# Kernel optimization log

Hardware: AMD Instinct MI355X
Metric: run time of the kernel (lower is better)

## Reference

```python
import jax, jax.numpy as jnp
import numpy as np

BN_EPS = 1e-5

def setup_inputs() -> dict:
    key = jax.random.key(0)
    k1, k2, k3 = jax.random.split(key, 3)
    N, T, C = 20000, 35, 4
    cin, cout = 7, 128
    h = cout // 2  # 64
    voxels = jax.random.normal(k1, (N, T, C), dtype=jnp.float32)
    # Linear params (torch default init scale ~ 1/sqrt(cin))
    W = jax.random.normal(k2, (h, cin), dtype=jnp.float32) / np.sqrt(cin)
    b = jax.random.normal(k3, (h,), dtype=jnp.float32) * 0.01
    gamma = jnp.ones((h,), dtype=jnp.float32)
    beta = jnp.zeros((h,), dtype=jnp.float32)
    return {"voxels": voxels, "W": W, "b": b, "gamma": gamma, "beta": beta}

def reference(voxels, W, b, gamma, beta):
    N, T, C = voxels.shape
    # mask of non-empty points: rows whose channel-sum is nonzero
    mask = (voxels.sum(axis=-1, keepdims=True) != 0)              # [N,T,1]
    counts = mask.sum(axis=1, keepdims=True).astype(voxels.dtype)  # [N,1,1]
    voxels_mean = voxels.sum(axis=1, keepdims=True) / counts       # [N,1,C]
    rel = voxels[:, :, :3] - voxels_mean[:, :, :3]                 # [N,T,3]
    aug = jnp.concatenate([voxels, rel], axis=-1)                  # [N,T,C+3]
    x = aug.reshape(-1, aug.shape[-1])                             # [N*T, 7]
    # Linear
    x = x @ W.T + b                                                # [N*T, h]
    # BatchNorm1d (training mode: batch stats, biased variance)
    mu = x.mean(axis=0)
    var = jnp.mean(jnp.square(x - mu), axis=0)
    x = (x - mu) / jnp.sqrt(var + BN_EPS) * gamma + beta
    # ReLU
    x = jnp.maximum(x, 0.0)
    x = x.reshape(N, T, -1)                                        # [N,T,h]
    agg = x.max(axis=1, keepdims=True)                             # [N,1,h]
    out = jnp.concatenate([x, jnp.broadcast_to(agg, x.shape)], axis=-1)  # [N,T,2h]
    return out
```

## Files before the change

### kernel.cpp

```cpp
#include <hip/hip_runtime.h>


#define NVOX   20000
#define TDIM   35
#define NCH    128
#define HID    64
#define NTF    700000.0f
#define EPS    1e-5f
#define NBLK_A 256
#define PARAM_OFF (NBLK_A * 35)

__global__ __launch_bounds__(256) void vfe_stats(const float* __restrict__ vox,
                                                 float* __restrict__ ws) {
  const int lane = threadIdx.x & 63;
  const int wid  = threadIdx.x >> 6;
  const int gwave  = (blockIdx.x * 256 + threadIdx.x) >> 6;
  const int nwaves = NBLK_A * 4;

  float m2[28], sv[7];
#pragma unroll
  for (int i = 0; i < 28; ++i) m2[i] = 0.f;
#pragma unroll
  for (int i = 0; i < 7; ++i) sv[i] = 0.f;

  for (int n = gwave; n < NVOX; n += nwaves) {
    float4 row = make_float4(0.f, 0.f, 0.f, 0.f);
    if (lane < TDIM) row = *(const float4*)(vox + (size_t)n * (TDIM * 4) + lane * 4);
    float rowsum = (row.x + row.y) + (row.z + row.w);
    float cnt = (float)__popcll(__ballot((lane < TDIM) && (rowsum != 0.f)));
    float s0 = row.x, s1 = row.y, s2 = row.z;
#pragma unroll
    for (int off = 32; off; off >>= 1) {
      s0 += __shfl_down(s0, off);
      s1 += __shfl_down(s1, off);
      s2 += __shfl_down(s2, off);
    }
    float rc = 1.f / cnt;
    float mx = __shfl(s0, 0) * rc;
    float my = __shfl(s1, 0) * rc;
    float mz = __shfl(s2, 0) * rc;
    if (lane < TDIM) {
      float a[7] = {row.x, row.y, row.z, row.w, row.x - mx, row.y - my, row.z - mz};
      int idx = 0;
#pragma unroll
      for (int j = 0; j < 7; ++j) {
        sv[j] += a[j];
#pragma unroll
        for (int k = j; k < 7; ++k) { m2[idx] = fmaf(a[j], a[k], m2[idx]); ++idx; }
      }
    }
  }

  __shared__ float part[4][35];
#pragma unroll
  for (int i = 0; i < 35; ++i) {
    float v = (i < 28) ? m2[i] : sv[i - 28];
#pragma unroll
    for (int off = 32; off; off >>= 1) v += __shfl_down(v, off);
    if (lane == 0) part[wid][i] = v;
  }
  __syncthreads();
  if (threadIdx.x < 35)
    ws[blockIdx.x * 35 + threadIdx.x] =
        part[0][threadIdx.x] + part[1][threadIdx.x] +
        part[2][threadIdx.x] + part[3][threadIdx.x];
}

__global__ void vfe_bnparams(const float* __restrict__ W, const float* __restrict__ b,
                             const float* __restrict__ gamma, const float* __restrict__ beta,
                             float* __restrict__ ws) {
  __shared__ float stats[35];
  for (int i = threadIdx.x; i < 35; i += 64) {
    float acc = 0.f;
    for (int p = 0; p < NBLK_A; ++p) acc += ws[p * 35 + i];
    stats[i] = acc;
  }
  __syncthreads();

  const int c = threadIdx.x;
  float m2[7][7];
  {
    int idx = 0;
    for (int j = 0; j < 7; ++j)
      for (int k = j; k < 7; ++k) { float v = stats[idx++]; m2[j][k] = v; m2[k][j] = v; }
  }
  float w[7];
#pragma unroll
  for (int j = 0; j < 7; ++j) w[j] = W[c * 7 + j];
  float bc = b[c];

  float wdots = 0.f;
#pragma unroll
  for (int j = 0; j < 7; ++j) wdots = fmaf(w[j], stats[28 + j], wdots);
  float q = 0.f;
#pragma unroll
  for (int j = 0; j < 7; ++j) {
    float t = 0.f;
#pragma unroll
    for (int k = 0; k < 7; ++k) t = fmaf(w[k], m2[j][k], t);
    q = fmaf(w[j], t, q);
  }
  float sx  = wdots + NTF * bc;
  float sxx = q + 2.f * bc * wdots + NTF * bc * bc;
  float mu  = sx / NTF;
  float var = sxx / NTF - mu * mu;
  float scale = gamma[c] / sqrtf(var + EPS);
  float shift = beta[c] + scale * (bc - mu);

  float* p = ws + PARAM_OFF + c * 8;
  p[0] = scale * (w[0] + w[4]);
  p[1] = scale * (w[1] + w[5]);
  p[2] = scale * (w[2] + w[6]);
  p[3] = scale * w[3];
  p[4] = scale * w[4];
  p[5] = scale * w[5];
  p[6] = scale * w[6];
  p[7] = shift;
}

__global__ __launch_bounds__(256) void vfe_encode(const float* __restrict__ vox,
                                                  const float* __restrict__ ws,
                                                  float* __restrict__ out) {
  const int lane = threadIdx.x & 63;
  const int wid  = threadIdx.x >> 6;
  const int n = (blockIdx.x * 256 + threadIdx.x) >> 6;

  __shared__ float4 rows[4][64];

  float4 row = make_float4(0.f, 0.f, 0.f, 0.f);
  if (lane < TDIM) row = *(const float4*)(vox + (size_t)n * (TDIM * 4) + lane * 4);
  float rowsum = (row.x + row.y) + (row.z + row.w);
  float cnt = (float)__popcll(__ballot((lane < TDIM) && (rowsum != 0.f)));
  float s0 = row.x, s1 = row.y, s2 = row.z;
#pragma unroll
  for (int off = 32; off; off >>= 1) {
    s0 += __shfl_down(s0, off);
    s1 += __shfl_down(s1, off);
    s2 += __shfl_down(s2, off);
  }
  float rc = 1.f / cnt;
  const float mx = __shfl(s0, 0) * rc;
  const float my = __shfl(s1, 0) * rc;
  const float mz = __shfl(s2, 0) * rc;

  rows[wid][lane] = row;
  __syncthreads();

  const int tg = lane >> 4;
  const int c4 = (lane & 15) << 2;

  const float4* pars = (const float4*)(ws + PARAM_OFF);
  float4 wv[4], wr[4];
  float base[4], agg[4];
#pragma unroll
  for (int i = 0; i < 4; ++i) {
    wv[i] = pars[(c4 + i) * 2];
    wr[i] = pars[(c4 + i) * 2 + 1];
    base[i] = wr[i].w - (wr[i].x * mx + wr[i].y * my + wr[i].z * mz);
    agg[i] = 0.f;
  }

  float* op = out + (size_t)n * (TDIM * NCH);
#pragma unroll
  for (int k = 0; k < 9; ++k) {
    const int t = 4 * k + tg;
    if (t < TDIM) {
      float4 v = rows[wid][t];
      float y[4];
#pragma unroll
      for (int i = 0; i < 4; ++i) {
        float d = fmaf(wv[i].x, v.x, base[i]);
        d = fmaf(wv[i].y, v.y, d);
        d = fmaf(wv[i].z, v.z, d);
        d = fmaf(wv[i].w, v.w, d);
        d = fmaxf(d, 0.f);
        agg[i] = fmaxf(agg[i], d);
        y[i] = d;
      }
      *(float4*)(op + t * NCH + c4) = make_float4(y[0], y[1], y[2], y[3]);
    }
  }

#pragma unroll
  for (int i = 0; i < 4; ++i) {
    agg[i] = fmaxf(agg[i], __shfl_xor(agg[i], 16));
    agg[i] = fmaxf(agg[i], __shfl_xor(agg[i], 32));
  }
  const float4 av = make_float4(agg[0], agg[1], agg[2], agg[3]);
#pragma unroll
  for (int k = 0; k < 9; ++k) {
    const int t = 4 * k + tg;
    if (t < TDIM) *(float4*)(op + t * NCH + HID + c4) = av;
  }
}

extern "C" void kernel_launch(void* const* d_in, const int* in_sizes, int n_in,
                              void* d_out, int out_size, void* d_ws, size_t ws_size,
                              hipStream_t stream) {
  const float* vox   = (const float*)d_in[0];
  const float* W     = (const float*)d_in[1];
  const float* b     = (const float*)d_in[2];
  const float* gamma = (const float*)d_in[3];
  const float* beta  = (const float*)d_in[4];
  float* out = (float*)d_out;
  float* ws  = (float*)d_ws;

  vfe_stats<<<NBLK_A, 256, 0, stream>>>(vox, ws);
  vfe_bnparams<<<1, 64, 0, stream>>>(W, b, gamma, beta, ws);
  vfe_encode<<<NVOX / 4, 256, 0, stream>>>(vox, ws, out);
}
```

Baseline: 407.7 us.

## Prefetch rows in stats loop, parallelize BN reduction, use nontemporal output stores

The stats kernel now software-prefetches the next voxel row while the current row is being processed, so load latency overlaps with compute. Partial statistics are stored transposed so the single-block bnparams kernel can reduce them with 280 threads using float4 loads, where before 35 threads did serial loops. The encode kernel writes its large output with nontemporal stores to avoid polluting the cache. The costs are extra registers for the prefetch and a dependence on how the hardware handles nontemporal stores.

```diff
diff --git a/kernel.cpp b/kernel.cpp
--- a/kernel.cpp
+++ b/kernel.cpp
@@ -10,6 +10,8 @@
 #define NBLK_A 256
 #define PARAM_OFF (NBLK_A * 35)
 
+typedef float nt4 __attribute__((ext_vector_type(4)));
+
 __global__ __launch_bounds__(256) void vfe_stats(const float* __restrict__ vox,
                                                  float* __restrict__ ws) {
   const int lane = threadIdx.x & 63;
@@ -23,9 +25,15 @@
 #pragma unroll
   for (int i = 0; i < 7; ++i) sv[i] = 0.f;
 
+  float4 row = make_float4(0.f, 0.f, 0.f, 0.f);
+  if (lane < TDIM) row = *(const float4*)(vox + (size_t)gwave * (TDIM * 4) + lane * 4);
+
   for (int n = gwave; n < NVOX; n += nwaves) {
-    float4 row = make_float4(0.f, 0.f, 0.f, 0.f);
-    if (lane < TDIM) row = *(const float4*)(vox + (size_t)n * (TDIM * 4) + lane * 4);
+    const int nn = n + nwaves;
+    float4 nxt = make_float4(0.f, 0.f, 0.f, 0.f);
+    if (nn < NVOX && lane < TDIM)
+      nxt = *(const float4*)(vox + (size_t)nn * (TDIM * 4) + lane * 4);
+
     float rowsum = (row.x + row.y) + (row.z + row.w);
     float cnt = (float)__popcll(__ballot((lane < TDIM) && (rowsum != 0.f)));
     float s0 = row.x, s1 = row.y, s2 = row.z;
@@ -49,6 +57,7 @@
         for (int k = j; k < 7; ++k) { m2[idx] = fmaf(a[j], a[k], m2[idx]); ++idx; }
       }
     }
+    row = nxt;
   }
 
   __shared__ float part[4][35];
@@ -61,23 +70,41 @@
   }
   __syncthreads();
   if (threadIdx.x < 35)
-    ws[blockIdx.x * 35 + threadIdx.x] =
+    ws[threadIdx.x * NBLK_A + blockIdx.x] =
         part[0][threadIdx.x] + part[1][threadIdx.x] +
         part[2][threadIdx.x] + part[3][threadIdx.x];
 }
 
-__global__ void vfe_bnparams(const float* __restrict__ W, const float* __restrict__ b,
+__global__ __launch_bounds__(320) void vfe_bnparams(const float* __restrict__ W,
+                             const float* __restrict__ b,
                              const float* __restrict__ gamma, const float* __restrict__ beta,
                              float* __restrict__ ws) {
+  __shared__ float part[35][8];
   __shared__ float stats[35];
-  for (int i = threadIdx.x; i < 35; i += 64) {
+  const int tid = threadIdx.x;
+
+  if (tid < 280) {
+    const int i = tid >> 3, g = tid & 7;
+    const float4* src = (const float4*)(ws + i * NBLK_A + g * 32);
     float acc = 0.f;
-    for (int p = 0; p < NBLK_A; ++p) acc += ws[p * 35 + i];
-    stats[i] = acc;
-  }
-  __syncthreads();
-
-  const int c = threadIdx.x;
+#pragma unroll
+    for (int q = 0; q < 8; ++q) {
+      float4 v = src[q];
+      acc += (v.x + v.y) + (v.z + v.w);
+    }
+    part[i][g] = acc;
+  }
+  __syncthreads();
+  if (tid < 35) {
+    float a = 0.f;
+#pragma unroll
+    for (int g = 0; g < 8; ++g) a += part[tid][g];
+    stats[tid] = a;
+  }
+  __syncthreads();
+  if (tid >= 64) return;
+
+  const int c = tid;
   float m2[7][7];
   {
     int idx = 0;
@@ -177,7 +204,8 @@
         agg[i] = fmaxf(agg[i], d);
         y[i] = d;
       }
-      *(float4*)(op + t * NCH + c4) = make_float4(y[0], y[1], y[2], y[3]);
+      nt4 yv = {y[0], y[1], y[2], y[3]};
+      __builtin_nontemporal_store(yv, (nt4*)(op + t * NCH + c4));
     }
   }
 
@@ -186,11 +214,12 @@
     agg[i] = fmaxf(agg[i], __shfl_xor(agg[i], 16));
     agg[i] = fmaxf(agg[i], __shfl_xor(agg[i], 32));
   }
-  const float4 av = make_float4(agg[0], agg[1], agg[2], agg[3]);
+  const nt4 av = {agg[0], agg[1], agg[2], agg[3]};
 #pragma unroll
   for (int k = 0; k < 9; ++k) {
     const int t = 4 * k + tg;
-    if (t < TDIM) *(float4*)(op + t * NCH + HID + c4) = av;
+    if (t < TDIM)
+      __builtin_nontemporal_store(av, (nt4*)(op + t * NCH + HID + c4));
   }
 }
 
@@ -206,6 +235,6 @@
   float* ws  = (float*)d_ws;
 
   vfe_stats<<<NBLK_A, 256, 0, stream>>>(vox, ws);
-  vfe_bnparams<<<1, 64, 0, stream>>>(W, b, gamma, beta, ws);
+  vfe_bnparams<<<1, 320, 0, stream>>>(W, b, gamma, beta, ws);
   vfe_encode<<<NVOX / 4, 256, 0, stream>>>(vox, ws, out);
 }
```

After: 389.4 us. -4.5%, faster.
